# Kernel optimization log

Hardware: AMD Instinct MI355X
Metric: run time of the kernel (lower is better)

Reference implementation:

```python
import jax, jax.numpy as jnp
import numpy as np
import math

B, S, D, H = 2, 2048, 1024, 16
DH = D // H
DFF = 4 * D
EPS = 1e-6


def layer_norm(x, g, b):
    # Faithful to the torch module: std is Bessel-corrected (ddof=1) and eps is
    # added to std (not variance).
    mean = jnp.mean(x, axis=-1, keepdims=True)
    var = jnp.sum((x - mean) ** 2, axis=-1, keepdims=True) / (x.shape[-1] - 1)
    return g * (x - mean) / (jnp.sqrt(var) + EPS) + b


def gelu_tanh(h):
    c = math.sqrt(2.0 / math.pi)
    return 0.5 * h * (1.0 + jnp.tanh(c * (h + 0.044715 * h ** 3)))


def attention(x, mask, wq, bq, wk, bk, wv, bv, wo, bo):
    b, s, d = x.shape
    q = (x @ wq + bq).reshape(b, s, H, DH)
    k = (x @ wk + bk).reshape(b, s, H, DH)
    v = (x @ wv + bv).reshape(b, s, H, DH)
    corr = jnp.einsum('bqhd,bkhd->bhqk', q, k) / math.sqrt(DH)  # [B,H,S,S]
    # original builds mask[:,None,:].repeat -> key-axis padding mask
    corr = jnp.where(mask[:, None, None, :] == 0, jnp.float32(-1e9), corr)
    prob = jax.nn.softmax(corr, axis=-1)
    hid = jnp.einsum('bhqk,bkhd->bqhd', prob, v).reshape(b, s, d)
    return hid @ wo + bo


def setup_inputs() -> dict:
    key = jax.random.key(0)
    ks = jax.random.split(key, 16)
    std = 0.02
    inp = {
        'hidden': jax.random.normal(ks[0], (B, S, D), jnp.float32),
        'mask': jax.random.randint(ks[1], (B, S), 0, 2, jnp.int32),
        'wq': jax.random.normal(ks[2], (D, D), jnp.float32) * std,
        'bq': jnp.zeros((D,), jnp.float32),
        'wk': jax.random.normal(ks[3], (D, D), jnp.float32) * std,
        'bk': jnp.zeros((D,), jnp.float32),
        'wv': jax.random.normal(ks[4], (D, D), jnp.float32) * std,
        'bv': jnp.zeros((D,), jnp.float32),
        'wo': jax.random.normal(ks[5], (D, D), jnp.float32) * std,
        'bo': jnp.zeros((D,), jnp.float32),
        'w1': jax.random.normal(ks[6], (D, DFF), jnp.float32) * std,
        'b1': jnp.zeros((DFF,), jnp.float32),
        'w2': jax.random.normal(ks[7], (DFF, D), jnp.float32) * std,
        'b2': jnp.zeros((D,), jnp.float32),
        'ln1_g': jnp.ones((D,), jnp.float32),
        'ln1_b': jnp.zeros((D,), jnp.float32),
        'ln2_g': jnp.ones((D,), jnp.float32),
        'ln2_b': jnp.zeros((D,), jnp.float32),
    }
    return inp


def reference(hidden, mask, wq, bq, wk, bk, wv, bv, wo, bo, w1, b1, w2, b2,
              ln1_g, ln1_b, ln2_g, ln2_b):
    # pre-norm residual attention sublayer (dropout = identity in eval)
    h = hidden + attention(layer_norm(hidden, ln1_g, ln1_b), mask,
                           wq, bq, wk, bk, wv, bv, wo, bo)
    # pre-norm residual FFN sublayer with tanh-GELU
    ff_in = layer_norm(h, ln2_g, ln2_b)
    h = h + (gelu_tanh(ff_in @ w1 + b1) @ w2 + b2)
    return h
```

## Files before the change

kernel.cpp:

```cpp
#include <hip/hip_runtime.h>

#define BB 2
#define SS 2048
#define DD 1024
#define HH 16
#define DHH 64
#define DFF 4096
#define MM (BB * SS)

typedef unsigned short u16;
typedef short short8 __attribute__((ext_vector_type(8)));
typedef float f32x4 __attribute__((ext_vector_type(4)));

__device__ __forceinline__ float b2f(u16 u) {
    return __uint_as_float(((unsigned)u) << 16);
}
__device__ __forceinline__ u16 f2b(float f) {
    unsigned u = __float_as_uint(f);
    unsigned r = (u + 0x7fffu + ((u >> 16) & 1u)) >> 16;
    return (u16)r;
}
__device__ __forceinline__ float gelu_tanh_f(float x) {
    float x3 = x * x * x;
    float t = 0.7978845608028654f * (x + 0.044715f * x3);
    return 0.5f * x * (1.0f + tanhf(t));
}
__device__ __forceinline__ void cp16(const u16* g, u16* l) {
    __builtin_amdgcn_global_load_lds(
        (const __attribute__((address_space(1))) void*)g,
        (__attribute__((address_space(3))) void*)l, 16, 0, 0);
}

__device__ __forceinline__ void wconv_tile(const float* __restrict__ W,
                                           u16* __restrict__ WT,
                                           int Kdim, int Ndim, int gk, int gn,
                                           float (*tile)[65], int t) {
    const int k0 = gk * 64, n0 = gn * 64;
    const int c = t & 63, r0 = (t >> 6) * 16;
#pragma unroll
    for (int i = 0; i < 16; ++i)
        tile[r0 + i][c] = W[(size_t)(k0 + r0 + i) * Ndim + n0 + c];
    __syncthreads();
    const int k4 = (t & 15) * 4, nr = t >> 4;
#pragma unroll
    for (int i = 0; i < 4; ++i) {
        int n = nr + 16 * i;
        ushort4 u = {f2b(tile[k4 + 0][n]), f2b(tile[k4 + 1][n]),
                     f2b(tile[k4 + 2][n]), f2b(tile[k4 + 3][n])};
        *(ushort4*)&WT[(size_t)(n0 + n) * Kdim + k0 + k4] = u;
    }
}

__global__ __launch_bounds__(256) void wconvA(const float* __restrict__ wq,
                                              const float* __restrict__ wk,
                                              const float* __restrict__ wv,
                                              const float* __restrict__ w2,
                                              u16* __restrict__ qkvT,
                                              u16* __restrict__ w2T) {
    __shared__ float tile[64][65];
    const int bid = blockIdx.x, t = threadIdx.x;
    if (bid < 768) {
        const int r = bid >> 8, li = bid & 255;
        const float* W = (r == 0) ? wq : ((r == 1) ? wk : wv);
        wconv_tile(W, qkvT + (size_t)r * 1048576, DD, DD, li & 15, li >> 4, tile, t);
    } else {
        const int li = bid - 768;
        wconv_tile(w2, w2T, DFF, DD, li & 63, li >> 6, tile, t);
    }
}

__global__ __launch_bounds__(256) void wconvB(const float* __restrict__ wo,
                                              const float* __restrict__ w1,
                                              u16* __restrict__ woT,
                                              u16* __restrict__ w1T) {
    __shared__ float tile[64][65];
    const int bid = blockIdx.x, t = threadIdx.x;
    if (bid < 256) {
        wconv_tile(wo, woT, DD, DD, bid & 15, bid >> 4, tile, t);
    } else {
        const int li = bid - 256;
        wconv_tile(w1, w1T, DD, DFF, li & 15, li >> 4, tile, t);
    }
}

__global__ __launch_bounds__(256) void pack3(const float* __restrict__ a,
                                             const float* __restrict__ b,
                                             const float* __restrict__ c,
                                             float* __restrict__ o) {
    int i = blockIdx.x * 256 + threadIdx.x;
    o[i] = (i < 1024) ? a[i] : ((i < 2048) ? b[i - 1024] : c[i - 2048]);
}

template <typename TI>
__global__ __launch_bounds__(256) void ln_kernel(const TI* __restrict__ x,
                                                 const float* __restrict__ g,
                                                 const float* __restrict__ bb,
                                                 u16* __restrict__ out) {
    __shared__ float red[8];
    const int row = blockIdx.x;
    const int t = threadIdx.x;
    const size_t base = (size_t)row * DD;

    float xv[4];
#pragma unroll
    for (int i = 0; i < 4; ++i) {
        int j = t + i * 256;
        if constexpr (sizeof(TI) == 2) xv[i] = b2f(((const u16*)x)[base + j]);
        else                            xv[i] = ((const float*)x)[base + j];
    }

    float part = xv[0] + xv[1] + xv[2] + xv[3];
#pragma unroll
    for (int off = 32; off > 0; off >>= 1) part += __shfl_xor(part, off);
    if ((t & 63) == 0) red[t >> 6] = part;
    __syncthreads();
    const float mean = (red[0] + red[1] + red[2] + red[3]) * (1.0f / 1024.0f);

    float dv[4];
#pragma unroll
    for (int i = 0; i < 4; ++i) dv[i] = xv[i] - mean;
    float p2 = dv[0] * dv[0] + dv[1] * dv[1] + dv[2] * dv[2] + dv[3] * dv[3];
#pragma unroll
    for (int off = 32; off > 0; off >>= 1) p2 += __shfl_xor(p2, off);
    if ((t & 63) == 0) red[4 + (t >> 6)] = p2;
    __syncthreads();
    const float var = (red[4] + red[5] + red[6] + red[7]) * (1.0f / 1023.0f);
    const float rden = 1.0f / (sqrtf(var) + 1e-6f);

#pragma unroll
    for (int i = 0; i < 4; ++i) {
        int j = t + i * 256;
        out[base + j] = f2b(g[j] * dv[i] * rden + bb[j]);
    }
}

template <int EPI>
__device__ __forceinline__ void gemm_store(int row, int col, float v,
                                           const void* res, void* out, int Ndim) {
    if (EPI == 0 || EPI == 4) {
        if (EPI == 4) v *= 0.125f;
        const int bq = row >> 11, ss = row & 2047;
        const int hh = col >> 6, dh = col & 63;
        ((u16*)out)[(((size_t)bq * HH + hh) * SS + ss) * DHH + dh] = f2b(v);
    } else if (EPI == 5) {
        const int reg = col >> 10, cc = col & 1023;
        if (reg == 0) v *= 0.125f;
        const int bq = row >> 11, ss = row & 2047;
        const int hh = cc >> 6, dh = cc & 63;
        ((u16*)out)[(size_t)reg * 4194304 +
                    (((size_t)bq * HH + hh) * SS + ss) * DHH + dh] = f2b(v);
    } else if (EPI == 1) {
        const size_t o = (size_t)row * Ndim + col;
        ((u16*)out)[o] = f2b(v + ((const float*)res)[o]);
    } else if (EPI == 2) {
        ((u16*)out)[(size_t)row * Ndim + col] = f2b(gelu_tanh_f(v));
    } else {
        const size_t o = (size_t)row * Ndim + col;
        ((float*)out)[o] = v + b2f(((const u16*)res)[o]);
    }
}

template <int EPI, int TM>
__global__ __launch_bounds__(256) void gemm_as(const u16* __restrict__ A,
                                               const u16* __restrict__ BTg,
                                               const float* __restrict__ bias,
                                               const void* __restrict__ res,
                                               void* __restrict__ out,
                                               int Ndim, int Kdim) {
    constexpr int NI = (TM == 128) ? 4 : 2;
    constexpr int NCA = TM / 32;
    __shared__ __align__(16) u16 As[TM * 64];
    __shared__ __align__(16) u16 Bs[128 * 64];

    const int t = threadIdx.x;
    const int w = t >> 6, l = t & 63;
    const int lm = l & 15, lg = l >> 4;
    const int m0 = blockIdx.y * TM, n0 = blockIdx.x * 128;
    const int wro = (TM == 128) ? (w >> 1) * 64 : 0;
    const int wco = (TM == 128) ? (w & 1) * 64 : w * 32;

    f32x4 acc[4][NI];
#pragma unroll
    for (int mi = 0; mi < 4; ++mi)
#pragma unroll
        for (int ni = 0; ni < NI; ++ni) acc[mi][ni] = (f32x4){0.f, 0.f, 0.f, 0.f};

    for (int k0 = 0; k0 < Kdim; k0 += 64) {
#pragma unroll
        for (int j = 0; j < NCA; ++j) {
            const int c = (w * NCA + j) * 64 + l;
            const int r = c >> 3, g = (c & 7) ^ (r & 7);
            cp16(A + (size_t)(m0 + r) * Kdim + k0 + g * 8,
                 &As[(w * NCA + j) * 512]);
        }
#pragma unroll
        for (int j = 0; j < 4; ++j) {
            const int c = (w * 4 + j) * 64 + l;
            const int r = c >> 3, g = (c & 7) ^ (r & 7);
            cp16(BTg + (size_t)(n0 + r) * Kdim + k0 + g * 8,
                 &Bs[(w * 4 + j) * 512]);
        }
        __syncthreads();

#pragma unroll
        for (int ks = 0; ks < 64; ks += 32) {
            short8 af[4], bf[NI];
#pragma unroll
            for (int mi = 0; mi < 4; ++mi) {
                const int row = wro + mi * 16 + lm;
                af[mi] = *(const short8*)&As[row * 64 + ((ks + lg * 8) ^ ((row & 7) * 8))];
            }
#pragma unroll
            for (int ni = 0; ni < NI; ++ni) {
                const int nn = wco + ni * 16 + lm;
                bf[ni] = *(const short8*)&Bs[nn * 64 + ((ks + lg * 8) ^ ((nn & 7) * 8))];
            }
#pragma unroll
            for (int mi = 0; mi < 4; ++mi)
#pragma unroll
                for (int ni = 0; ni < NI; ++ni)
                    acc[mi][ni] = __builtin_amdgcn_mfma_f32_16x16x32_bf16(
                        af[mi], bf[ni], acc[mi][ni], 0, 0, 0);
        }
        __syncthreads();
    }

#pragma unroll
    for (int ni = 0; ni < NI; ++ni) {
        const int col = n0 + wco + ni * 16 + lm;
        const float bv = bias[col];
#pragma unroll
        for (int mi = 0; mi < 4; ++mi)
#pragma unroll
            for (int r = 0; r < 4; ++r)
                gemm_store<EPI>(m0 + wro + mi * 16 + lg * 4 + r, col,
                                acc[mi][ni][r] + bv, res, out, Ndim);
    }
}

template <int EPI, int TM>
__global__ __launch_bounds__(256) void gemm_fb(const u16* __restrict__ A,
                                               const float* __restrict__ W,
                                               const float* __restrict__ bias,
                                               const void* __restrict__ res,
                                               void* __restrict__ out,
                                               int Ndim, int Kdim) {
    constexpr int NI = (TM == 128) ? 4 : 2;
    __shared__ __align__(16) u16 As[TM * 64];
    __shared__ __align__(16) u16 BT[128 * 64];

    const int t = threadIdx.x;
    const int w = t >> 6, l = t & 63;
    const int lm = l & 15, lg = l >> 4;
    const int m0 = blockIdx.y * TM, n0 = blockIdx.x * 128;
    const int wro = (TM == 128) ? (w >> 1) * 64 : 0;
    const int wco = (TM == 128) ? (w & 1) * 64 : w * 32;

    f32x4 acc[4][NI];
#pragma unroll
    for (int mi = 0; mi < 4; ++mi)
#pragma unroll
        for (int ni = 0; ni < NI; ++ni) acc[mi][ni] = (f32x4){0.f, 0.f, 0.f, 0.f};

    const int bn = t & 127;
    const int bk4 = (t >> 7) * 4;

    for (int k0 = 0; k0 < Kdim; k0 += 64) {
#pragma unroll
        for (int it = 0; it < TM / 32; ++it) {
            int idx = it * 256 + t;
            int row = idx >> 3, c8 = (idx & 7) * 8;
            short8 v = *(const short8*)(A + (size_t)(m0 + row) * Kdim + k0 + c8);
            *(short8*)&As[row * 64 + (c8 ^ ((row & 7) * 8))] = v;
        }
#pragma unroll
        for (int it = 0; it < 8; ++it) {
            int kq = it * 8 + bk4;
            const float* wp = W + (size_t)(k0 + kq) * Ndim + n0 + bn;
            ushort4 u = {f2b(wp[0]), f2b(wp[(size_t)Ndim]),
                         f2b(wp[2 * (size_t)Ndim]), f2b(wp[3 * (size_t)Ndim])};
            *(ushort4*)&BT[bn * 64 + (kq ^ ((bn & 7) * 8))] = u;
        }
        __syncthreads();

#pragma unroll
        for (int ks = 0; ks < 64; ks += 32) {
            short8 af[4], bf[NI];
#pragma unroll
            for (int mi = 0; mi < 4; ++mi) {
                const int row = wro + mi * 16 + lm;
                af[mi] = *(const short8*)&As[row * 64 + ((ks + lg * 8) ^ ((row & 7) * 8))];
            }
#pragma unroll
            for (int ni = 0; ni < NI; ++ni) {
                const int nn = wco + ni * 16 + lm;
                bf[ni] = *(const short8*)&BT[nn * 64 + ((ks + lg * 8) ^ ((nn & 7) * 8))];
            }
#pragma unroll
            for (int mi = 0; mi < 4; ++mi)
#pragma unroll
                for (int ni = 0; ni < NI; ++ni)
                    acc[mi][ni] = __builtin_amdgcn_mfma_f32_16x16x32_bf16(
                        af[mi], bf[ni], acc[mi][ni], 0, 0, 0);
        }
        __syncthreads();
    }

#pragma unroll
    for (int ni = 0; ni < NI; ++ni) {
        const int col = n0 + wco + ni * 16 + lm;
        const float bv = bias[col];
#pragma unroll
        for (int mi = 0; mi < 4; ++mi)
#pragma unroll
            for (int r = 0; r < 4; ++r)
                gemm_store<EPI>(m0 + wro + mi * 16 + lg * 4 + r, col,
                                acc[mi][ni][r] + bv, res, out, Ndim);
    }
}

__global__ __launch_bounds__(256) void attn_split(const u16* __restrict__ qg,
                                                  const u16* __restrict__ kg,
                                                  const u16* __restrict__ vg,
                                                  const int* __restrict__ mask,
                                                  u16* __restrict__ p0,
                                                  u16* __restrict__ p1,
                                                  float* __restrict__ sume_g) {
    __shared__ __align__(16) u16 Ks[64 * 72];
    __shared__ __align__(16) u16 VTs[64 * 72];
    __shared__ __align__(16) float maskf[64];

    const int t = threadIdx.x;
    const int w = t >> 6;
    const int l = t & 63;
    const int lm = l & 15, lg = l >> 4;
    const int h = blockIdx.y;
    const int z = blockIdx.z;
    const int b = z >> 1, half = z & 1;
    const int qbase = blockIdx.x * 128 + w * 32;
    const size_t bhS = ((size_t)b * HH + h) * SS;
    u16* pO = half ? p1 : p0;
    const int kt0 = half * (SS / 2);

    short8 qlo[2], qhi[2];
#pragma unroll
    for (int qp = 0; qp < 2; ++qp) {
        const u16* qrow = qg + (bhS + qbase + qp * 16 + lm) * DHH + lg * 8;
        qlo[qp] = *(const short8*)qrow;
        qhi[qp] = *(const short8*)(qrow + 32);
    }

    f32x4 acc[2][4];
#pragma unroll
    for (int qp = 0; qp < 2; ++qp)
#pragma unroll
        for (int i = 0; i < 4; ++i) acc[qp][i] = (f32x4){0.f, 0.f, 0.f, 0.f};
    float sume[2] = {0.f, 0.f};

    const int kq = (t & 15) * 4, dq = (t >> 4) * 4;

    for (int kt = kt0; kt < kt0 + SS / 2; kt += 64) {
        __syncthreads();
#pragma unroll
        for (int it = 0; it < 4; ++it) {
            int idx = it * 256 + t;
            int row = idx >> 4, c4 = (idx & 15) * 4;
            ushort4 u = *(const ushort4*)(kg + (bhS + kt + row) * DHH + c4);
            *(ushort4*)&Ks[row * 72 + c4] = u;
        }
        {
            ushort4 a0 = *(const ushort4*)(vg + (bhS + kt + kq + 0) * DHH + dq);
            ushort4 a1 = *(const ushort4*)(vg + (bhS + kt + kq + 1) * DHH + dq);
            ushort4 a2 = *(const ushort4*)(vg + (bhS + kt + kq + 2) * DHH + dq);
            ushort4 a3 = *(const ushort4*)(vg + (bhS + kt + kq + 3) * DHH + dq);
            ushort4 w0 = {a0.x, a1.x, a2.x, a3.x};
            ushort4 w1 = {a0.y, a1.y, a2.y, a3.y};
            ushort4 w2 = {a0.z, a1.z, a2.z, a3.z};
            ushort4 w3 = {a0.w, a1.w, a2.w, a3.w};
            *(ushort4*)&VTs[(dq + 0) * 72 + kq] = w0;
            *(ushort4*)&VTs[(dq + 1) * 72 + kq] = w1;
            *(ushort4*)&VTs[(dq + 2) * 72 + kq] = w2;
            *(ushort4*)&VTs[(dq + 3) * 72 + kq] = w3;
        }
        if (t < 64) maskf[t] = mask[b * SS + kt + t] ? 1.0f : 0.0f;
        __syncthreads();

#pragma unroll
        for (int kb = 0; kb < 64; kb += 32) {
            short8 kfa[2], kfc[2];
#pragma unroll
            for (int s = 0; s < 2; ++s) {
                const int keyrow = kb + 8 * (lm >> 2) + 4 * s + (lm & 3);
                const u16* kr = &Ks[keyrow * 72 + lg * 8];
                kfa[s] = *(const short8*)kr;
                kfc[s] = *(const short8*)(kr + 32);
            }
            short8 p8[2];
#pragma unroll
            for (int qp = 0; qp < 2; ++qp) {
                float ev[8];
#pragma unroll
                for (int s = 0; s < 2; ++s) {
                    f32x4 c = (f32x4){0.f, 0.f, 0.f, 0.f};
                    c = __builtin_amdgcn_mfma_f32_16x16x32_bf16(kfa[s], qlo[qp], c, 0, 0, 0);
                    c = __builtin_amdgcn_mfma_f32_16x16x32_bf16(kfc[s], qhi[qp], c, 0, 0, 0);
                    const float4 mv = *(const float4*)&maskf[kb + 8 * lg + 4 * s];
                    float e0 = __expf(c[0]) * mv.x;
                    float e1 = __expf(c[1]) * mv.y;
                    float e2 = __expf(c[2]) * mv.z;
                    float e3 = __expf(c[3]) * mv.w;
                    sume[qp] += e0 + e1 + e2 + e3;
                    ev[4 * s + 0] = e0; ev[4 * s + 1] = e1;
                    ev[4 * s + 2] = e2; ev[4 * s + 3] = e3;
                }
#pragma unroll
                for (int i = 0; i < 8; ++i)
                    p8[qp][i] = (short)(__float_as_uint(ev[i]) >> 16);
            }
#pragma unroll
            for (int d0 = 0; d0 < 4; ++d0) {
                const short8 v8 = *(const short8*)&VTs[(d0 * 16 + lm) * 72 + kb + lg * 8];
#pragma unroll
                for (int qp = 0; qp < 2; ++qp)
                    acc[qp][d0] = __builtin_amdgcn_mfma_f32_16x16x32_bf16(
                        p8[qp], v8, acc[qp][d0], 0, 0, 0);
            }
        }
    }

#pragma unroll
    for (int qp = 0; qp < 2; ++qp) {
        float s = sume[qp];
        s += __shfl_xor(s, 16);
        s += __shfl_xor(s, 32);
        if (l < 16)
            sume_g[(size_t)half * (BB * HH * SS) + bhS + qbase + qp * 16 + lm] = s;
#pragma unroll
        for (int d0 = 0; d0 < 4; ++d0)
#pragma unroll
            for (int r = 0; r < 4; ++r) {
                const int q = qbase + qp * 16 + 4 * lg + r;
                pO[(size_t)(b * SS + q) * DD + h * DHH + d0 * 16 + lm] =
                    f2b(acc[qp][d0][r]);
            }
    }
}

__global__ __launch_bounds__(256) void attn_merge(const u16* __restrict__ p1,
                                                  const float* __restrict__ sume_g,
                                                  u16* __restrict__ hid) {
    const int row = blockIdx.x;
    const int b = row >> 11, s = row & 2047;
    const int t = threadIdx.x;
#pragma unroll
    for (int i = 0; i < 4; ++i) {
        const int j = t + i * 256;
        const int h = j >> 6;
        const size_t si = ((size_t)b * HH + h) * SS + s;
        const float d = sume_g[si] + sume_g[(size_t)BB * HH * SS + si];
        const size_t o = (size_t)row * DD + j;
        hid[o] = f2b((b2f(hid[o]) + b2f(p1[o])) / d);
    }
}

__global__ __launch_bounds__(256) void attn_mfma2(const u16* __restrict__ qg,
                                                  const u16* __restrict__ kg,
                                                  const u16* __restrict__ vg,
                                                  const int* __restrict__ mask,
                                                  u16* __restrict__ hid) {
    __shared__ __align__(16) u16 Ks[64 * 72];
    __shared__ __align__(16) u16 VTs[64 * 72];
    __shared__ __align__(16) float maskf[64];

    const int t = threadIdx.x;
    const int w = t >> 6;
    const int l = t & 63;
    const int lm = l & 15, lg = l >> 4;
    const int h = blockIdx.y, b = blockIdx.z;
    const int qbase = blockIdx.x * 128 + w * 32;
    const size_t bhS = ((size_t)b * HH + h) * SS;

    short8 qlo[2], qhi[2];
#pragma unroll
    for (int qp = 0; qp < 2; ++qp) {
        const u16* qrow = qg + (bhS + qbase + qp * 16 + lm) * DHH + lg * 8;
        qlo[qp] = *(const short8*)qrow;
        qhi[qp] = *(const short8*)(qrow + 32);
    }

    f32x4 acc[2][4];
#pragma unroll
    for (int qp = 0; qp < 2; ++qp)
#pragma unroll
        for (int i = 0; i < 4; ++i) acc[qp][i] = (f32x4){0.f, 0.f, 0.f, 0.f};
    float sume[2] = {0.f, 0.f};

    const int kq = (t & 15) * 4, dq = (t >> 4) * 4;

    for (int kt = 0; kt < SS; kt += 64) {
        __syncthreads();
#pragma unroll
        for (int it = 0; it < 4; ++it) {
            int idx = it * 256 + t;
            int row = idx >> 4, c4 = (idx & 15) * 4;
            ushort4 u = *(const ushort4*)(kg + (bhS + kt + row) * DHH + c4);
            *(ushort4*)&Ks[row * 72 + c4] = u;
        }
        {
            ushort4 a0 = *(const ushort4*)(vg + (bhS + kt + kq + 0) * DHH + dq);
            ushort4 a1 = *(const ushort4*)(vg + (bhS + kt + kq + 1) * DHH + dq);
            ushort4 a2 = *(const ushort4*)(vg + (bhS + kt + kq + 2) * DHH + dq);
            ushort4 a3 = *(const ushort4*)(vg + (bhS + kt + kq + 3) * DHH + dq);
            ushort4 w0 = {a0.x, a1.x, a2.x, a3.x};
            ushort4 w1 = {a0.y, a1.y, a2.y, a3.y};
            ushort4 w2 = {a0.z, a1.z, a2.z, a3.z};
            ushort4 w3 = {a0.w, a1.w, a2.w, a3.w};
            *(ushort4*)&VTs[(dq + 0) * 72 + kq] = w0;
            *(ushort4*)&VTs[(dq + 1) * 72 + kq] = w1;
            *(ushort4*)&VTs[(dq + 2) * 72 + kq] = w2;
            *(ushort4*)&VTs[(dq + 3) * 72 + kq] = w3;
        }
        if (t < 64) maskf[t] = mask[b * SS + kt + t] ? 1.0f : 0.0f;
        __syncthreads();

#pragma unroll
        for (int kb = 0; kb < 64; kb += 32) {
            short8 kfa[2], kfc[2];
#pragma unroll
            for (int s = 0; s < 2; ++s) {
                const int keyrow = kb + 8 * (lm >> 2) + 4 * s + (lm & 3);
                const u16* kr = &Ks[keyrow * 72 + lg * 8];
                kfa[s] = *(const short8*)kr;
                kfc[s] = *(const short8*)(kr + 32);
            }
            short8 p8[2];
#pragma unroll
            for (int qp = 0; qp < 2; ++qp) {
                float ev[8];
#pragma unroll
                for (int s = 0; s < 2; ++s) {
                    f32x4 c = (f32x4){0.f, 0.f, 0.f, 0.f};
                    c = __builtin_amdgcn_mfma_f32_16x16x32_bf16(kfa[s], qlo[qp], c, 0, 0, 0);
                    c = __builtin_amdgcn_mfma_f32_16x16x32_bf16(kfc[s], qhi[qp], c, 0, 0, 0);
                    const float4 mv = *(const float4*)&maskf[kb + 8 * lg + 4 * s];
                    float e0 = __expf(c[0]) * mv.x;
                    float e1 = __expf(c[1]) * mv.y;
                    float e2 = __expf(c[2]) * mv.z;
                    float e3 = __expf(c[3]) * mv.w;
                    sume[qp] += e0 + e1 + e2 + e3;
                    ev[4 * s + 0] = e0; ev[4 * s + 1] = e1;
                    ev[4 * s + 2] = e2; ev[4 * s + 3] = e3;
                }
#pragma unroll
                for (int i = 0; i < 8; ++i)
                    p8[qp][i] = (short)(__float_as_uint(ev[i]) >> 16);
            }
#pragma unroll
            for (int d0 = 0; d0 < 4; ++d0) {
                const short8 v8 = *(const short8*)&VTs[(d0 * 16 + lm) * 72 + kb + lg * 8];
#pragma unroll
                for (int qp = 0; qp < 2; ++qp)
                    acc[qp][d0] = __builtin_amdgcn_mfma_f32_16x16x32_bf16(
                        p8[qp], v8, acc[qp][d0], 0, 0, 0);
            }
        }
    }

#pragma unroll
    for (int qp = 0; qp < 2; ++qp) {
        float s = sume[qp];
        s += __shfl_xor(s, 16);
        s += __shfl_xor(s, 32);
        float rinv[4];
#pragma unroll
        for (int r = 0; r < 4; ++r) rinv[r] = 1.0f / __shfl(s, 4 * lg + r);
#pragma unroll
        for (int d0 = 0; d0 < 4; ++d0)
#pragma unroll
            for (int r = 0; r < 4; ++r) {
                const int q = qbase + qp * 16 + 4 * lg + r;
                hid[(size_t)(b * SS + q) * DD + h * DHH + d0 * 16 + lm] =
                    f2b(acc[qp][d0][r] * rinv[r]);
            }
    }
}

extern "C" void kernel_launch(void* const* d_in, const int* in_sizes, int n_in,
                              void* d_out, int out_size, void* d_ws, size_t ws_size,
                              hipStream_t stream) {
    (void)in_sizes; (void)n_in; (void)out_size;

    const float* hidden = (const float*)d_in[0];
    const int*   mask   = (const int*)d_in[1];
    const float* wq = (const float*)d_in[2];  const float* bq = (const float*)d_in[3];
    const float* wk = (const float*)d_in[4];  const float* bk = (const float*)d_in[5];
    const float* wv = (const float*)d_in[6];  const float* bv = (const float*)d_in[7];
    const float* wo = (const float*)d_in[8];  const float* bo = (const float*)d_in[9];
    const float* w1 = (const float*)d_in[10]; const float* b1 = (const float*)d_in[11];
    const float* w2 = (const float*)d_in[12]; const float* b2 = (const float*)d_in[13];
    const float* ln1g = (const float*)d_in[14]; const float* ln1b = (const float*)d_in[15];
    const float* ln2g = (const float*)d_in[16]; const float* ln2b = (const float*)d_in[17];

    char* ws = (char*)d_ws;
    u16* R0 = (u16*)(ws + 0);
    u16* R1 = (u16*)(ws + 8388608);
    u16* R2 = (u16*)(ws + 16777216);
    u16* R3 = (u16*)(ws + 25165824);
    float* outp = (float*)d_out;

    const size_t WTOFF = 33554432;
    const bool big = ws_size >= WTOFF + 25165824 + 16384;

    if (big) {
        u16* qkvT = (u16*)(ws + WTOFF);
        u16* woT  = (u16*)(ws + WTOFF + 6291456);
        u16* w1T  = (u16*)(ws + WTOFF + 8388608);
        u16* w2T  = (u16*)(ws + WTOFF + 16777216);
        float* bqkv = (float*)(ws + WTOFF + 25165824);
        u16* p1 = w1T;
        float* sume_g = (float*)d_out;

        wconvA<<<1792, 256, 0, stream>>>(wq, wk, wv, w2, qkvT, w2T);
        pack3<<<12, 256, 0, stream>>>(bq, bk, bv, bqkv);

        ln_kernel<float><<<MM, 256, 0, stream>>>(hidden, ln1g, ln1b, R0);
        gemm_as<5, 128><<<dim3(3072 / 128, MM / 128), 256, 0, stream>>>(
            R0, qkvT, bqkv, nullptr, R1, 3072, DD);
        attn_split<<<dim3(SS / 128, HH, BB * 2), 256, 0, stream>>>(
            R1, R2, R3, mask, R0, p1, sume_g);
        attn_merge<<<MM, 256, 0, stream>>>(p1, sume_g, R0);
        wconvB<<<1280, 256, 0, stream>>>(wo, w1, woT, w1T);
        gemm_as<1, 128><<<dim3(DD / 128, MM / 128), 256, 0, stream>>>(
            R0, woT, bo, hidden, R3, DD, DD);
        ln_kernel<u16><<<MM, 256, 0, stream>>>(R3, ln2g, ln2b, R0);
        for (int s2 = 0; s2 < 2; ++s2) {
            const size_t r0 = (size_t)s2 * 2048;
            gemm_as<2, 128><<<dim3(DFF / 128, 2048 / 128), 256, 0, stream>>>(
                R0 + r0 * DD, w1T, b1, nullptr, R1, DFF, DD);
            gemm_as<3, 64><<<dim3(DD / 128, 2048 / 64), 256, 0, stream>>>(
                R1, w2T, b2, R3 + r0 * DD, outp + r0 * DD, DD, DFF);
        }
    } else {
        ln_kernel<float><<<MM, 256, 0, stream>>>(hidden, ln1g, ln1b, R0);
        gemm_fb<4, 128><<<dim3(DD / 128, MM / 128), 256, 0, stream>>>(R0, wq, bq, nullptr, R1, DD, DD);
        gemm_fb<0, 128><<<dim3(DD / 128, MM / 128), 256, 0, stream>>>(R0, wk, bk, nullptr, R2, DD, DD);
        gemm_fb<0, 128><<<dim3(DD / 128, MM / 128), 256, 0, stream>>>(R0, wv, bv, nullptr, R3, DD, DD);
        attn_mfma2<<<dim3(SS / 128, HH, BB), 256, 0, stream>>>(R1, R2, R3, mask, R0);
        gemm_fb<1, 128><<<dim3(DD / 128, MM / 128), 256, 0, stream>>>(R0, wo, bo, hidden, R3, DD, DD);
        ln_kernel<u16><<<MM, 256, 0, stream>>>(R3, ln2g, ln2b, R0);
        for (int s2 = 0; s2 < 2; ++s2) {
            const size_t r0 = (size_t)s2 * 2048;
            gemm_fb<2, 128><<<dim3(DFF / 128, 2048 / 128), 256, 0, stream>>>(
                R0 + r0 * DD, w1, b1, nullptr, R1, DFF, DD);
            gemm_fb<3, 64><<<dim3(DD / 128, 2048 / 64), 256, 0, stream>>>(
                R1, w2, b2, R3 + r0 * DD, outp + r0 * DD, DD, DFF);
        }
    }
}
```

Baseline: 492.9 us.

## Rewrite split attention to read K/V-transposed from global, fold mask and log2e into scores

The QKV GEMM epilogue now stores V transposed per head and pre-scales Q by log2(e)/sqrt(DH), and a precomputed additive mask bias is packed alongside the biases. The new split-attention kernel reads K and V^T fragments directly from global memory without LDS staging or barriers. It seeds the score accumulator with the mask bias, uses exp2, and computes row sums with an MFMA against a ones vector. The generic GEMM also gains a TN parameter, so the Wo and W2 GEMMs use 64-wide N tiles for more blocks. The cost is more global traffic per wave, and the -10000 mask bias only approximates the reference's -1e9 masking.

```diff
diff --git a/kernel.cpp b/kernel.cpp
--- a/kernel.cpp
+++ b/kernel.cpp
@@ -83,12 +83,19 @@
     }
 }
 
-__global__ __launch_bounds__(256) void pack3(const float* __restrict__ a,
-                                             const float* __restrict__ b,
-                                             const float* __restrict__ c,
-                                             float* __restrict__ o) {
+__global__ __launch_bounds__(256) void pack_misc(const float* __restrict__ a,
+                                                 const float* __restrict__ b,
+                                                 const float* __restrict__ c,
+                                                 const int* __restrict__ mask,
+                                                 float* __restrict__ o,
+                                                 float* __restrict__ maskb) {
     int i = blockIdx.x * 256 + threadIdx.x;
-    o[i] = (i < 1024) ? a[i] : ((i < 2048) ? b[i - 1024] : c[i - 2048]);
+    if (i < 3072) {
+        o[i] = (i < 1024) ? a[i] : ((i < 2048) ? b[i - 1024] : c[i - 2048]);
+    } else {
+        int j = i - 3072;
+        maskb[j] = mask[j] ? 0.0f : -10000.0f;
+    }
 }
 
 template <typename TI>
@@ -144,11 +151,16 @@
         ((u16*)out)[(((size_t)bq * HH + hh) * SS + ss) * DHH + dh] = f2b(v);
     } else if (EPI == 5) {
         const int reg = col >> 10, cc = col & 1023;
-        if (reg == 0) v *= 0.125f;
         const int bq = row >> 11, ss = row & 2047;
         const int hh = cc >> 6, dh = cc & 63;
-        ((u16*)out)[(size_t)reg * 4194304 +
-                    (((size_t)bq * HH + hh) * SS + ss) * DHH + dh] = f2b(v);
+        if (reg == 2) {
+            ((u16*)out)[(size_t)2 * 4194304 +
+                        (((size_t)bq * HH + hh) * DHH + dh) * SS + ss] = f2b(v);
+        } else {
+            if (reg == 0) v *= 0.18033688011112042f;
+            ((u16*)out)[(size_t)reg * 4194304 +
+                        (((size_t)bq * HH + hh) * SS + ss) * DHH + dh] = f2b(v);
+        }
     } else if (EPI == 1) {
         const size_t o = (size_t)row * Ndim + col;
         ((u16*)out)[o] = f2b(v + ((const float*)res)[o]);
@@ -160,28 +172,28 @@
     }
 }
 
-template <int EPI, int TM>
+template <int EPI, int TM, int TN>
 __global__ __launch_bounds__(256) void gemm_as(const u16* __restrict__ A,
                                                const u16* __restrict__ BTg,
                                                const float* __restrict__ bias,
                                                const void* __restrict__ res,
                                                void* __restrict__ out,
                                                int Ndim, int Kdim) {
-    constexpr int NI = (TM == 128) ? 4 : 2;
-    constexpr int NCA = TM / 32;
+    constexpr int MI = TM / 32, NI = TN / 32;
+    constexpr int NCA = TM / 32, NCB = TN / 32;
     __shared__ __align__(16) u16 As[TM * 64];
-    __shared__ __align__(16) u16 Bs[128 * 64];
+    __shared__ __align__(16) u16 Bs[TN * 64];
 
     const int t = threadIdx.x;
     const int w = t >> 6, l = t & 63;
     const int lm = l & 15, lg = l >> 4;
-    const int m0 = blockIdx.y * TM, n0 = blockIdx.x * 128;
-    const int wro = (TM == 128) ? (w >> 1) * 64 : 0;
-    const int wco = (TM == 128) ? (w & 1) * 64 : w * 32;
-
-    f32x4 acc[4][NI];
-#pragma unroll
-    for (int mi = 0; mi < 4; ++mi)
+    const int m0 = blockIdx.y * TM, n0 = blockIdx.x * TN;
+    const int wro = (w >> 1) * (TM / 2);
+    const int wco = (w & 1) * (TN / 2);
+
+    f32x4 acc[MI][NI];
+#pragma unroll
+    for (int mi = 0; mi < MI; ++mi)
 #pragma unroll
         for (int ni = 0; ni < NI; ++ni) acc[mi][ni] = (f32x4){0.f, 0.f, 0.f, 0.f};
 
@@ -194,19 +206,19 @@
                  &As[(w * NCA + j) * 512]);
         }
 #pragma unroll
-        for (int j = 0; j < 4; ++j) {
-            const int c = (w * 4 + j) * 64 + l;
+        for (int j = 0; j < NCB; ++j) {
+            const int c = (w * NCB + j) * 64 + l;
             const int r = c >> 3, g = (c & 7) ^ (r & 7);
             cp16(BTg + (size_t)(n0 + r) * Kdim + k0 + g * 8,
-                 &Bs[(w * 4 + j) * 512]);
+                 &Bs[(w * NCB + j) * 512]);
         }
         __syncthreads();
 
 #pragma unroll
         for (int ks = 0; ks < 64; ks += 32) {
-            short8 af[4], bf[NI];
-#pragma unroll
-            for (int mi = 0; mi < 4; ++mi) {
+            short8 af[MI], bf[NI];
+#pragma unroll
+            for (int mi = 0; mi < MI; ++mi) {
                 const int row = wro + mi * 16 + lm;
                 af[mi] = *(const short8*)&As[row * 64 + ((ks + lg * 8) ^ ((row & 7) * 8))];
             }
@@ -216,7 +228,7 @@
                 bf[ni] = *(const short8*)&Bs[nn * 64 + ((ks + lg * 8) ^ ((nn & 7) * 8))];
             }
 #pragma unroll
-            for (int mi = 0; mi < 4; ++mi)
+            for (int mi = 0; mi < MI; ++mi)
 #pragma unroll
                 for (int ni = 0; ni < NI; ++ni)
                     acc[mi][ni] = __builtin_amdgcn_mfma_f32_16x16x32_bf16(
@@ -230,7 +242,7 @@
         const int col = n0 + wco + ni * 16 + lm;
         const float bv = bias[col];
 #pragma unroll
-        for (int mi = 0; mi < 4; ++mi)
+        for (int mi = 0; mi < MI; ++mi)
 #pragma unroll
             for (int r = 0; r < 4; ++r)
                 gemm_store<EPI>(m0 + wro + mi * 16 + lg * 4 + r, col,
@@ -319,23 +331,17 @@
     }
 }
 
-__global__ __launch_bounds__(256) void attn_split(const u16* __restrict__ qg,
-                                                  const u16* __restrict__ kg,
-                                                  const u16* __restrict__ vg,
-                                                  const int* __restrict__ mask,
-                                                  u16* __restrict__ p0,
-                                                  u16* __restrict__ p1,
-                                                  float* __restrict__ sume_g) {
-    __shared__ __align__(16) u16 Ks[64 * 72];
-    __shared__ __align__(16) u16 VTs[64 * 72];
-    __shared__ __align__(16) float maskf[64];
-
+__global__ __launch_bounds__(256) void attn_gl(const u16* __restrict__ qg,
+                                               const u16* __restrict__ kg,
+                                               const u16* __restrict__ vtg,
+                                               const float* __restrict__ maskb,
+                                               u16* __restrict__ p0,
+                                               u16* __restrict__ p1,
+                                               float* __restrict__ sume_g) {
     const int t = threadIdx.x;
-    const int w = t >> 6;
-    const int l = t & 63;
+    const int w = t >> 6, l = t & 63;
     const int lm = l & 15, lg = l >> 4;
-    const int h = blockIdx.y;
-    const int z = blockIdx.z;
+    const int h = blockIdx.y, z = blockIdx.z;
     const int b = z >> 1, half = z & 1;
     const int qbase = blockIdx.x * 128 + w * 32;
     const size_t bhS = ((size_t)b * HH + h) * SS;
@@ -350,6 +356,124 @@
         qhi[qp] = *(const short8*)(qrow + 32);
     }
 
+    const u16* kbase = kg + (bhS + kt0 + 8 * (lm >> 2) + (lm & 3)) * DHH + lg * 8;
+    const u16* vbase = vtg + (((size_t)b * HH + h) * DHH + lm) * SS + kt0 + lg * 8;
+    const float* mbase = maskb + b * SS + kt0 + 8 * lg;
+
+    f32x4 acc[2][4];
+#pragma unroll
+    for (int qp = 0; qp < 2; ++qp)
+#pragma unroll
+        for (int i = 0; i < 4; ++i) acc[qp][i] = (f32x4){0.f, 0.f, 0.f, 0.f};
+    f32x4 accs[2] = {(f32x4){0.f, 0.f, 0.f, 0.f}, (f32x4){0.f, 0.f, 0.f, 0.f}};
+
+    short8 ones;
+#pragma unroll
+    for (int i = 0; i < 8; ++i) ones[i] = (short)0x3F80;
+
+    for (int kt = 0; kt < SS / 2; kt += 32) {
+        const u16* kr0 = kbase + (size_t)kt * DHH;
+        const u16* kr1 = kbase + (size_t)(kt + 4) * DHH;
+        const short8 kfa0 = *(const short8*)kr0;
+        const short8 kfc0 = *(const short8*)(kr0 + 32);
+        const short8 kfa1 = *(const short8*)kr1;
+        const short8 kfc1 = *(const short8*)(kr1 + 32);
+        const float4 mb0 = *(const float4*)(mbase + kt);
+        const float4 mb1 = *(const float4*)(mbase + kt + 4);
+        short8 v8[4];
+#pragma unroll
+        for (int d0 = 0; d0 < 4; ++d0)
+            v8[d0] = *(const short8*)(vbase + (size_t)d0 * 16 * SS + kt);
+
+        short8 p8[2];
+#pragma unroll
+        for (int qp = 0; qp < 2; ++qp) {
+            f32x4 c0 = (f32x4){mb0.x, mb0.y, mb0.z, mb0.w};
+            c0 = __builtin_amdgcn_mfma_f32_16x16x32_bf16(kfa0, qlo[qp], c0, 0, 0, 0);
+            c0 = __builtin_amdgcn_mfma_f32_16x16x32_bf16(kfc0, qhi[qp], c0, 0, 0, 0);
+            f32x4 c1 = (f32x4){mb1.x, mb1.y, mb1.z, mb1.w};
+            c1 = __builtin_amdgcn_mfma_f32_16x16x32_bf16(kfa1, qlo[qp], c1, 0, 0, 0);
+            c1 = __builtin_amdgcn_mfma_f32_16x16x32_bf16(kfc1, qhi[qp], c1, 0, 0, 0);
+            float ev[8];
+#pragma unroll
+            for (int i = 0; i < 4; ++i) ev[i] = exp2f(c0[i]);
+#pragma unroll
+            for (int i = 0; i < 4; ++i) ev[4 + i] = exp2f(c1[i]);
+#pragma unroll
+            for (int i = 0; i < 8; ++i)
+                p8[qp][i] = (short)(__float_as_uint(ev[i]) >> 16);
+            accs[qp] = __builtin_amdgcn_mfma_f32_16x16x32_bf16(
+                p8[qp], ones, accs[qp], 0, 0, 0);
+        }
+#pragma unroll
+        for (int d0 = 0; d0 < 4; ++d0)
+#pragma unroll
+            for (int qp = 0; qp < 2; ++qp)
+                acc[qp][d0] = __builtin_amdgcn_mfma_f32_16x16x32_bf16(
+                    p8[qp], v8[d0], acc[qp][d0], 0, 0, 0);
+    }
+
+#pragma unroll
+    for (int qp = 0; qp < 2; ++qp) {
+        if (lm == 0) {
+#pragma unroll
+            for (int r = 0; r < 4; ++r)
+                sume_g[(size_t)half * (BB * HH * SS) + bhS +
+                       qbase + qp * 16 + 4 * lg + r] = accs[qp][r];
+        }
+#pragma unroll
+        for (int d0 = 0; d0 < 4; ++d0)
+#pragma unroll
+            for (int r = 0; r < 4; ++r) {
+                const int q = qbase + qp * 16 + 4 * lg + r;
+                pO[(size_t)(b * SS + q) * DD + h * DHH + d0 * 16 + lm] =
+                    f2b(acc[qp][d0][r]);
+            }
+    }
+}
+
+__global__ __launch_bounds__(256) void attn_merge(const u16* __restrict__ p1,
+                                                  const float* __restrict__ sume_g,
+                                                  u16* __restrict__ hid) {
+    const int row = blockIdx.x;
+    const int b = row >> 11, s = row & 2047;
+    const int t = threadIdx.x;
+#pragma unroll
+    for (int i = 0; i < 4; ++i) {
+        const int j = t + i * 256;
+        const int h = j >> 6;
+        const size_t si = ((size_t)b * HH + h) * SS + s;
+        const float d = sume_g[si] + sume_g[(size_t)BB * HH * SS + si];
+        const size_t o = (size_t)row * DD + j;
+        hid[o] = f2b((b2f(hid[o]) + b2f(p1[o])) / d);
+    }
+}
+
+__global__ __launch_bounds__(256) void attn_mfma2(const u16* __restrict__ qg,
+                                                  const u16* __restrict__ kg,
+                                                  const u16* __restrict__ vg,
+                                                  const int* __restrict__ mask,
+                                                  u16* __restrict__ hid) {
+    __shared__ __align__(16) u16 Ks[64 * 72];
+    __shared__ __align__(16) u16 VTs[64 * 72];
+    __shared__ __align__(16) float maskf[64];
+
+    const int t = threadIdx.x;
+    const int w = t >> 6;
+    const int l = t & 63;
+    const int lm = l & 15, lg = l >> 4;
+    const int h = blockIdx.y, b = blockIdx.z;
+    const int qbase = blockIdx.x * 128 + w * 32;
+    const size_t bhS = ((size_t)b * HH + h) * SS;
+
+    short8 qlo[2], qhi[2];
+#pragma unroll
+    for (int qp = 0; qp < 2; ++qp) {
+        const u16* qrow = qg + (bhS + qbase + qp * 16 + lm) * DHH + lg * 8;
+        qlo[qp] = *(const short8*)qrow;
+        qhi[qp] = *(const short8*)(qrow + 32);
+    }
+
     f32x4 acc[2][4];
 #pragma unroll
     for (int qp = 0; qp < 2; ++qp)
@@ -359,7 +483,7 @@
 
     const int kq = (t & 15) * 4, dq = (t >> 4) * 4;
 
-    for (int kt = kt0; kt < kt0 + SS / 2; kt += 64) {
+    for (int kt = 0; kt < SS; kt += 64) {
         __syncthreads();
 #pragma unroll
         for (int it = 0; it < 4; ++it) {
@@ -433,144 +557,6 @@
         float s = sume[qp];
         s += __shfl_xor(s, 16);
         s += __shfl_xor(s, 32);
-        if (l < 16)
-            sume_g[(size_t)half * (BB * HH * SS) + bhS + qbase + qp * 16 + lm] = s;
-#pragma unroll
-        for (int d0 = 0; d0 < 4; ++d0)
-#pragma unroll
-            for (int r = 0; r < 4; ++r) {
-                const int q = qbase + qp * 16 + 4 * lg + r;
-                pO[(size_t)(b * SS + q) * DD + h * DHH + d0 * 16 + lm] =
-                    f2b(acc[qp][d0][r]);
-            }
-    }
-}
-
-__global__ __launch_bounds__(256) void attn_merge(const u16* __restrict__ p1,
-                                                  const float* __restrict__ sume_g,
-                                                  u16* __restrict__ hid) {
-    const int row = blockIdx.x;
-    const int b = row >> 11, s = row & 2047;
-    const int t = threadIdx.x;
-#pragma unroll
-    for (int i = 0; i < 4; ++i) {
-        const int j = t + i * 256;
-        const int h = j >> 6;
-        const size_t si = ((size_t)b * HH + h) * SS + s;
-        const float d = sume_g[si] + sume_g[(size_t)BB * HH * SS + si];
-        const size_t o = (size_t)row * DD + j;
-        hid[o] = f2b((b2f(hid[o]) + b2f(p1[o])) / d);
-    }
-}
-
-__global__ __launch_bounds__(256) void attn_mfma2(const u16* __restrict__ qg,
-                                                  const u16* __restrict__ kg,
-                                                  const u16* __restrict__ vg,
-                                                  const int* __restrict__ mask,
-                                                  u16* __restrict__ hid) {
-    __shared__ __align__(16) u16 Ks[64 * 72];
-    __shared__ __align__(16) u16 VTs[64 * 72];
-    __shared__ __align__(16) float maskf[64];
-
-    const int t = threadIdx.x;
-    const int w = t >> 6;
-    const int l = t & 63;
-    const int lm = l & 15, lg = l >> 4;
-    const int h = blockIdx.y, b = blockIdx.z;
-    const int qbase = blockIdx.x * 128 + w * 32;
-    const size_t bhS = ((size_t)b * HH + h) * SS;
-
-    short8 qlo[2], qhi[2];
-#pragma unroll
-    for (int qp = 0; qp < 2; ++qp) {
-        const u16* qrow = qg + (bhS + qbase + qp * 16 + lm) * DHH + lg * 8;
-        qlo[qp] = *(const short8*)qrow;
-        qhi[qp] = *(const short8*)(qrow + 32);
-    }
-
-    f32x4 acc[2][4];
-#pragma unroll
-    for (int qp = 0; qp < 2; ++qp)
-#pragma unroll
-        for (int i = 0; i < 4; ++i) acc[qp][i] = (f32x4){0.f, 0.f, 0.f, 0.f};
-    float sume[2] = {0.f, 0.f};
-
-    const int kq = (t & 15) * 4, dq = (t >> 4) * 4;
-
-    for (int kt = 0; kt < SS; kt += 64) {
-        __syncthreads();
-#pragma unroll
-        for (int it = 0; it < 4; ++it) {
-            int idx = it * 256 + t;
-            int row = idx >> 4, c4 = (idx & 15) * 4;
-            ushort4 u = *(const ushort4*)(kg + (bhS + kt + row) * DHH + c4);
-            *(ushort4*)&Ks[row * 72 + c4] = u;
-        }
-        {
-            ushort4 a0 = *(const ushort4*)(vg + (bhS + kt + kq + 0) * DHH + dq);
-            ushort4 a1 = *(const ushort4*)(vg + (bhS + kt + kq + 1) * DHH + dq);
-            ushort4 a2 = *(const ushort4*)(vg + (bhS + kt + kq + 2) * DHH + dq);
-            ushort4 a3 = *(const ushort4*)(vg + (bhS + kt + kq + 3) * DHH + dq);
-            ushort4 w0 = {a0.x, a1.x, a2.x, a3.x};
-            ushort4 w1 = {a0.y, a1.y, a2.y, a3.y};
-            ushort4 w2 = {a0.z, a1.z, a2.z, a3.z};
-            ushort4 w3 = {a0.w, a1.w, a2.w, a3.w};
-            *(ushort4*)&VTs[(dq + 0) * 72 + kq] = w0;
-            *(ushort4*)&VTs[(dq + 1) * 72 + kq] = w1;
-            *(ushort4*)&VTs[(dq + 2) * 72 + kq] = w2;
-            *(ushort4*)&VTs[(dq + 3) * 72 + kq] = w3;
-        }
-        if (t < 64) maskf[t] = mask[b * SS + kt + t] ? 1.0f : 0.0f;
-        __syncthreads();
-
-#pragma unroll
-        for (int kb = 0; kb < 64; kb += 32) {
-            short8 kfa[2], kfc[2];
-#pragma unroll
-            for (int s = 0; s < 2; ++s) {
-                const int keyrow = kb + 8 * (lm >> 2) + 4 * s + (lm & 3);
-                const u16* kr = &Ks[keyrow * 72 + lg * 8];
-                kfa[s] = *(const short8*)kr;
-                kfc[s] = *(const short8*)(kr + 32);
-            }
-            short8 p8[2];
-#pragma unroll
-            for (int qp = 0; qp < 2; ++qp) {
-                float ev[8];
-#pragma unroll
-                for (int s = 0; s < 2; ++s) {
-                    f32x4 c = (f32x4){0.f, 0.f, 0.f, 0.f};
-                    c = __builtin_amdgcn_mfma_f32_16x16x32_bf16(kfa[s], qlo[qp], c, 0, 0, 0);
-                    c = __builtin_amdgcn_mfma_f32_16x16x32_bf16(kfc[s], qhi[qp], c, 0, 0, 0);
-                    const float4 mv = *(const float4*)&maskf[kb + 8 * lg + 4 * s];
-                    float e0 = __expf(c[0]) * mv.x;
-                    float e1 = __expf(c[1]) * mv.y;
-                    float e2 = __expf(c[2]) * mv.z;
-                    float e3 = __expf(c[3]) * mv.w;
-                    sume[qp] += e0 + e1 + e2 + e3;
-                    ev[4 * s + 0] = e0; ev[4 * s + 1] = e1;
-                    ev[4 * s + 2] = e2; ev[4 * s + 3] = e3;
-                }
-#pragma unroll
-                for (int i = 0; i < 8; ++i)
-                    p8[qp][i] = (short)(__float_as_uint(ev[i]) >> 16);
-            }
-#pragma unroll
-            for (int d0 = 0; d0 < 4; ++d0) {
-                const short8 v8 = *(const short8*)&VTs[(d0 * 16 + lm) * 72 + kb + lg * 8];
-#pragma unroll
-                for (int qp = 0; qp < 2; ++qp)
-                    acc[qp][d0] = __builtin_amdgcn_mfma_f32_16x16x32_bf16(
-                        p8[qp], v8, acc[qp][d0], 0, 0, 0);
-            }
-        }
-    }
-
-#pragma unroll
-    for (int qp = 0; qp < 2; ++qp) {
-        float s = sume[qp];
-        s += __shfl_xor(s, 16);
-        s += __shfl_xor(s, 32);
         float rinv[4];
 #pragma unroll
         for (int r = 0; r < 4; ++r) rinv[r] = 1.0f / __shfl(s, 4 * lg + r);
@@ -609,35 +595,36 @@
     float* outp = (float*)d_out;
 
     const size_t WTOFF = 33554432;
-    const bool big = ws_size >= WTOFF + 25165824 + 16384;
+    const bool big = ws_size >= WTOFF + 25165824 + 32768;
 
     if (big) {
         u16* qkvT = (u16*)(ws + WTOFF);
         u16* woT  = (u16*)(ws + WTOFF + 6291456);
         u16* w1T  = (u16*)(ws + WTOFF + 8388608);
         u16* w2T  = (u16*)(ws + WTOFF + 16777216);
-        float* bqkv = (float*)(ws + WTOFF + 25165824);
+        float* bqkv  = (float*)(ws + WTOFF + 25165824);
+        float* maskb = (float*)(ws + WTOFF + 25165824 + 12288);
         u16* p1 = w1T;
         float* sume_g = (float*)d_out;
 
         wconvA<<<1792, 256, 0, stream>>>(wq, wk, wv, w2, qkvT, w2T);
-        pack3<<<12, 256, 0, stream>>>(bq, bk, bv, bqkv);
+        pack_misc<<<28, 256, 0, stream>>>(bq, bk, bv, mask, bqkv, maskb);
 
         ln_kernel<float><<<MM, 256, 0, stream>>>(hidden, ln1g, ln1b, R0);
-        gemm_as<5, 128><<<dim3(3072 / 128, MM / 128), 256, 0, stream>>>(
+        gemm_as<5, 128, 128><<<dim3(3072 / 128, MM / 128), 256, 0, stream>>>(
             R0, qkvT, bqkv, nullptr, R1, 3072, DD);
-        attn_split<<<dim3(SS / 128, HH, BB * 2), 256, 0, stream>>>(
-            R1, R2, R3, mask, R0, p1, sume_g);
+        attn_gl<<<dim3(SS / 128, HH, BB * 2), 256, 0, stream>>>(
+            R1, R2, R3, maskb, R0, p1, sume_g);
         attn_merge<<<MM, 256, 0, stream>>>(p1, sume_g, R0);
         wconvB<<<1280, 256, 0, stream>>>(wo, w1, woT, w1T);
-        gemm_as<1, 128><<<dim3(DD / 128, MM / 128), 256, 0, stream>>>(
+        gemm_as<1, 128, 64><<<dim3(DD / 64, MM / 128), 256, 0, stream>>>(
             R0, woT, bo, hidden, R3, DD, DD);
         ln_kernel<u16><<<MM, 256, 0, stream>>>(R3, ln2g, ln2b, R0);
         for (int s2 = 0; s2 < 2; ++s2) {
             const size_t r0 = (size_t)s2 * 2048;
-            gemm_as<2, 128><<<dim3(DFF / 128, 2048 / 128), 256, 0, stream>>>(
+            gemm_as<2, 128, 128><<<dim3(DFF / 128, 2048 / 128), 256, 0, stream>>>(
                 R0 + r0 * DD, w1T, b1, nullptr, R1, DFF, DD);
-            gemm_as<3, 64><<<dim3(DD / 128, 2048 / 64), 256, 0, stream>>>(
+            gemm_as<3, 64, 64><<<dim3(DD / 64, 2048 / 64), 256, 0, stream>>>(
                 R1, w2T, b2, R3 + r0 * DD, outp + r0 * DD, DD, DFF);
         }
     } else {
```

New measurement: 509.7 us. +3.4%, slower.
